# Performance work log

Measured on AMD Instinct MI355X. Metric: run time of the kernel, lower is better.

Reference implementation:

```python
import jax, jax.numpy as jnp
import numpy as np

H = 16          # n_heads
DH = 128        # head_dim
DR = 64         # rope_dim
DC = DH - DR    # content_dim = 64
THETA = 10000.0
SCALE = 1.0 / np.sqrt(DH)


def _rope_tables(T, dtype):
    inv = 1.0 / (THETA ** (jnp.arange(0, DR, 2, dtype=jnp.float32) / DR))  # [DR/2]
    t = jnp.arange(T, dtype=jnp.float32)
    freqs = jnp.outer(t, inv)  # [T, DR/2]
    return jnp.cos(freqs).astype(dtype), jnp.sin(freqs).astype(dtype)


def _apply_rope(x, cos, sin):
    # x: [B,H,T,DR]; cos/sin: [T,DR/2] broadcast over B,H
    d = x.shape[-1] // 2
    x1, x2 = x[..., :d], x[..., d:]
    return jnp.concatenate([x1 * cos - x2 * sin, x1 * sin + x2 * cos], axis=-1)


def setup_inputs() -> dict:
    key = jax.random.key(0)
    ks = jax.random.split(key, 9)
    B, T, D = 1, 2048, 2048
    s = 0.02
    return {
        "x": jax.random.normal(ks[0], (B, T, D), jnp.float32),
        "Wq_down": jax.random.normal(ks[1], (D, 512), jnp.float32) * s,
        "Wq_up": jax.random.normal(ks[2], (512, H * DC), jnp.float32) * s,
        "Wq_rope": jax.random.normal(ks[3], (D, H * DR), jnp.float32) * s,
        "Wkv_down": jax.random.normal(ks[4], (D, 512), jnp.float32) * s,
        "Wk_up": jax.random.normal(ks[5], (512, H * DC), jnp.float32) * s,
        "Wv_up": jax.random.normal(ks[6], (512, H * DH), jnp.float32) * s,
        "Wk_rope": jax.random.normal(ks[7], (D, H * DR), jnp.float32) * s,
        "Wo": jax.random.normal(ks[8], (H * DH, D), jnp.float32) * s,
    }


def reference(x, Wq_down, Wq_up, Wq_rope, Wkv_down, Wk_up, Wv_up, Wk_rope, Wo):
    B, T, D = x.shape
    # low-rank query path: down then up, content part only
    q_content = ((x @ Wq_down) @ Wq_up).reshape(B, T, H, DC).transpose(0, 2, 1, 3)
    q_pos = (x @ Wq_rope).reshape(B, T, H, DR).transpose(0, 2, 1, 3)
    kv_latent = x @ Wkv_down                    # [B,T,d_latent]
    k_pos = (x @ Wk_rope).reshape(B, T, H, DR).transpose(0, 2, 1, 3)

    cos, sin = _rope_tables(T, x.dtype)
    q_pos = _apply_rope(q_pos, cos, sin)
    k_pos = _apply_rope(k_pos, cos, sin)

    k_content = (kv_latent @ Wk_up).reshape(B, T, H, DC).transpose(0, 2, 1, 3)
    v = (kv_latent @ Wv_up).reshape(B, T, H, DH).transpose(0, 2, 1, 3)

    q = jnp.concatenate([q_content, q_pos], axis=-1)  # [B,H,T,DH]
    k = jnp.concatenate([k_content, k_pos], axis=-1)  # [B,H,T,DH]

    scores = jnp.einsum("bhtd,bhsd->bhts", q, k) * SCALE
    causal = jnp.tril(jnp.ones((T, T), dtype=bool))
    scores = jnp.where(causal, scores, jnp.finfo(scores.dtype).min)
    attn = jax.nn.softmax(scores, axis=-1)
    out = jnp.einsum("bhts,bhsd->bhtd", attn, v)       # [B,H,T,DH]
    out = out.transpose(0, 2, 1, 3).reshape(B, T, H * DH)
    return out @ Wo
```

## Files before the change

### kernel.cpp

```cpp
#include <hip/hip_runtime.h>
#include <math.h>

#define T_SEQ 2048
#define D_MODEL 2048
#define H_HEADS 16
#define DH 128
#define DR 64
#define DC 64
#define D_LAT 512
#define NSPLIT 3
#define QSCALE (0.08838834764831845f * 1.4426950408889634f)

typedef __attribute__((ext_vector_type(8))) short short8;
typedef __attribute__((ext_vector_type(4))) short short4v;
typedef __attribute__((ext_vector_type(4))) float f32x4;

__device__ __forceinline__ float bf2f(short b) {
    unsigned u = ((unsigned)(unsigned short)b) << 16;
    return __builtin_bit_cast(float, u);
}
__device__ __forceinline__ short f2bf(float f) {
    unsigned u = __builtin_bit_cast(unsigned, f);
    unsigned r = u + 0x7fffu + ((u >> 16) & 1u);
    return (short)(r >> 16);
}
__device__ __forceinline__ short f2bf_trunc(float f) {
    return (short)(__builtin_bit_cast(unsigned, f) >> 16);
}

#define GLD_LDS(gp, lp) \
    __builtin_amdgcn_global_load_lds( \
        (const __attribute__((address_space(1))) void*)(gp), \
        (__attribute__((address_space(3))) void*)(lp), 16, 0, 0)

__device__ __forceinline__ void ct_tile(float (*tile)[33],
                                        const float* __restrict__ W,
                                        short* __restrict__ Wt,
                                        int R, int C, int ldo, int rel) {
    int bx = rel % (C / 32), by = rel / (C / 32);
    int c0 = bx * 32, r0 = by * 32;
    int tx = threadIdx.x & 31, ty = threadIdx.x >> 5;
    #pragma unroll
    for (int i = 0; i < 4; ++i)
        tile[ty + i * 8][tx] = W[(size_t)(r0 + ty + i * 8) * C + c0 + tx];
    __syncthreads();
    #pragma unroll
    for (int i = 0; i < 4; ++i)
        Wt[(size_t)(c0 + ty + i * 8) * ldo + r0 + tx] = f2bf(tile[tx][ty + i * 8]);
    __syncthreads();
}

__global__ __launch_bounds__(256) void prep(const float* __restrict__ x,
                                            short* __restrict__ xb,
                                            const float* __restrict__ Wqd,
                                            const float* __restrict__ Wkvd,
                                            const float* __restrict__ Wqr,
                                            const float* __restrict__ Wkr,
                                            const float* __restrict__ Wqu,
                                            const float* __restrict__ Wku,
                                            const float* __restrict__ Wvu,
                                            const float* __restrict__ Wo,
                                            short* __restrict__ WdT,
                                            short* __restrict__ WupT2,
                                            short* __restrict__ WoT) {
    __shared__ float tile[32][33];
    int bid = blockIdx.x;
    if (bid < 4096) {
        int i = bid * 1024 + threadIdx.x * 4;
        float4 f = *(const float4*)&x[i];
        short4v o;
        o.x = f2bf(f.x); o.y = f2bf(f.y); o.z = f2bf(f.z); o.w = f2bf(f.w);
        *(short4v*)&xb[i] = o;
    } else if (bid < 5120) {
        ct_tile(tile, Wqd,  WdT + (size_t)0 * 2048,    2048, 512,  2048, bid - 4096);
    } else if (bid < 6144) {
        ct_tile(tile, Wkvd, WdT + (size_t)512 * 2048,  2048, 512,  2048, bid - 5120);
    } else if (bid < 8192) {
        ct_tile(tile, Wqr,  WdT + (size_t)1024 * 2048, 2048, 1024, 2048, bid - 6144);
    } else if (bid < 10240) {
        ct_tile(tile, Wkr,  WdT + (size_t)2048 * 2048, 2048, 1024, 2048, bid - 8192);
    } else if (bid < 10752) {
        ct_tile(tile, Wqu,  WupT2 + (size_t)0 * 512,    512, 1024, 512, bid - 10240);
    } else if (bid < 11264) {
        ct_tile(tile, Wku,  WupT2 + (size_t)1024 * 512, 512, 1024, 512, bid - 10752);
    } else if (bid < 12288) {
        ct_tile(tile, Wvu,  WupT2 + (size_t)2048 * 512, 512, 2048, 512, bid - 11264);
    } else {
        ct_tile(tile, Wo,   WoT, 2048, 2048, 2048, bid - 12288);
    }
}

__global__ __launch_bounds__(256) void transpose_bf16(const short* __restrict__ in,
                                                      short* __restrict__ outb,
                                                      int ldi) {
    __shared__ short tile[64][65];
    int c0 = blockIdx.x * 64, t0 = blockIdx.y * 64;
    int tx = threadIdx.x & 31, ty = threadIdx.x >> 5;
    #pragma unroll
    for (int i = 0; i < 8; ++i) {
        int r = ty + i * 8;
        int vv = *(const int*)&in[(size_t)(t0 + r) * ldi + c0 + tx * 2];
        tile[r][tx * 2]     = (short)(vv & 0xffff);
        tile[r][tx * 2 + 1] = (short)(((unsigned)vv) >> 16);
    }
    __syncthreads();
    #pragma unroll
    for (int i = 0; i < 8; ++i) {
        int c = ty + i * 8;
        unsigned lo = (unsigned short)tile[tx * 2][c];
        unsigned hi = (unsigned short)tile[tx * 2 + 1][c];
        *(int*)&outb[(size_t)(c0 + c) * 2048 + t0 + tx * 2] = (int)(lo | (hi << 16));
    }
}

__global__ __launch_bounds__(256) void gemm_bt(const short* __restrict__ A,
                                               const short* __restrict__ A2,
                                               const short* __restrict__ Bt,
                                               short* __restrict__ C0,
                                               short* __restrict__ C1,
                                               int M, int N, int Kblk,
                                               int lda, int ldb, int ldc,
                                               int ncut, int scut, float cscale) {
    __shared__ short As[128 * 32];
    __shared__ short Bs[128 * 32];
    const int tid = threadIdx.x;
    const int wave = tid >> 6, lane = tid & 63;
    const int row0 = blockIdx.y * 128, col0 = blockIdx.x * 128;
    const int kbase = blockIdx.z * Kblk;
    const short* Ause = (col0 < ncut) ? A : A2;
    short* Cuse = blockIdx.z ? C1 : C0;
    const int wr = (wave >> 1) * 64, wc = (wave & 1) * 64;
    const int lr = lane & 15, quad = lane >> 4;

    f32x4 acc[4][4];
    #pragma unroll
    for (int i = 0; i < 4; ++i)
        #pragma unroll
        for (int j = 0; j < 4; ++j) acc[i][j] = (f32x4){0.f, 0.f, 0.f, 0.f};

    for (int k0 = kbase; k0 < kbase + Kblk; k0 += 32) {
        __syncthreads();
        #pragma unroll
        for (int it = 0; it < 2; ++it) {
            int idx = wave * 64 + it * 256 + lane;
            const short* ga = Ause + (size_t)(row0 + (idx >> 2)) * lda + k0 + (idx & 3) * 8;
            const short* gb = Bt   + (size_t)(col0 + (idx >> 2)) * ldb + k0 + (idx & 3) * 8;
            int lds0 = (wave * 64 + it * 256) * 8;
            GLD_LDS(ga, &As[lds0]);
            GLD_LDS(gb, &Bs[lds0]);
        }
        __syncthreads();

        short8 af[4], bfr[4];
        #pragma unroll
        for (int i = 0; i < 4; ++i)
            af[i] = *(const short8*)&As[(wr + i * 16 + lr) * 32 + quad * 8];
        #pragma unroll
        for (int j = 0; j < 4; ++j)
            bfr[j] = *(const short8*)&Bs[(wc + j * 16 + lr) * 32 + quad * 8];
        #pragma unroll
        for (int i = 0; i < 4; ++i)
            #pragma unroll
            for (int j = 0; j < 4; ++j)
                acc[i][j] = __builtin_amdgcn_mfma_f32_16x16x32_bf16(af[i], bfr[j],
                                                                   acc[i][j], 0, 0, 0);
    }

    const float sc = (col0 < scut) ? cscale : 1.0f;
    #pragma unroll
    for (int i = 0; i < 4; ++i) {
        int rb = row0 + wr + i * 16 + quad * 4;
        #pragma unroll
        for (int j = 0; j < 4; ++j) {
            int c = col0 + wc + j * 16 + lr;
            #pragma unroll
            for (int r = 0; r < 4; ++r)
                Cuse[(size_t)(rb + r) * ldc + c] = f2bf(acc[i][j][r] * sc);
        }
    }
}

__global__ __launch_bounds__(256) void add_bf16(short* __restrict__ a,
                                                const short* __restrict__ b) {
    int i = (blockIdx.x * 256 + threadIdx.x) * 8;
    short8 av = *(const short8*)&a[i];
    short8 bv = *(const short8*)&b[i];
    short8 o;
    #pragma unroll
    for (int j = 0; j < 8; ++j) o[j] = f2bf(bf2f(av[j]) + bf2f(bv[j]));
    *(short8*)&a[i] = o;
}

__global__ __launch_bounds__(256) void add_out_f32(const short* __restrict__ p0,
                                                   const short* __restrict__ p1,
                                                   float* __restrict__ out) {
    int i = (blockIdx.x * 256 + threadIdx.x) * 4;
    short4v a = *(const short4v*)&p0[i];
    short4v b = *(const short4v*)&p1[i];
    float4 o;
    o.x = bf2f(a.x) + bf2f(b.x);
    o.y = bf2f(a.y) + bf2f(b.y);
    o.z = bf2f(a.z) + bf2f(b.z);
    o.w = bf2f(a.w) + bf2f(b.w);
    *(float4*)&out[i] = o;
}

__global__ __launch_bounds__(256) void rope_cat(short* __restrict__ cat) {
    int idx = blockIdx.x * 256 + threadIdx.x;
    int i = idx & 31;
    int h = (idx >> 5) & (H_HEADS - 1);
    int t = (idx >> 9) & (T_SEQ - 1);
    int which = idx >> 20;
    size_t base = (size_t)t * 3072 + 1024 + which * 1024 + h * DR;
    float x1 = bf2f(cat[base + i]);
    float x2 = bf2f(cat[base + 32 + i]);
    float freq = (float)t * __powf(10000.0f, -(float)i / 32.0f);
    float c = cosf(freq), s = sinf(freq);
    float sc = which ? 1.0f : QSCALE;
    cat[base + i]      = f2bf((x1 * c - x2 * s) * sc);
    cat[base + 32 + i] = f2bf((x1 * s + x2 * c) * sc);
}

__global__ __launch_bounds__(256) void attn_mla_split(const short* __restrict__ qkup,
                                                      const short* __restrict__ cat,
                                                      const short* __restrict__ vT,
                                                      short* __restrict__ Opart01,
                                                      short* __restrict__ Opart2,
                                                      float* __restrict__ lpart) {
    const int p = blockIdx.x;
    const int h = blockIdx.y;
    const int g = blockIdx.z;
    const int tid = threadIdx.x;
    const int wave = tid >> 6, lane = tid & 63;
    const int lr = lane & 15, quad = lane >> 4;

    __shared__ short Ks[32 * 128];
    __shared__ short Vst[128 * 32];
    __shared__ short Ps[4][16 * 40];

    short* Og = (g < 2) ? Opart01 + (size_t)g * (T_SEQ * 2048) : Opart2;
    const short8 ones = {0x3F80, 0x3F80, 0x3F80, 0x3F80,
                         0x3F80, 0x3F80, 0x3F80, 0x3F80};

    for (int rep = 0; rep < 2; ++rep) {
        const int qt = rep ? (31 - p) : p;
        const int Q0 = qt * 64;
        const int qrow0 = Q0 + wave * 16;
        const int nchunk = 2 * qt + 2;
        const int qmax = qrow0 + 15;

        short8 qf[4];
        {
            int t = qrow0 + lr;
            #pragma unroll
            for (int kci = 0; kci < 4; ++kci) {
                const short* src = (kci < 2)
                    ? qkup + (size_t)t * 4096 + h * 64
                    : cat + (size_t)t * 3072 + 1024 + h * 64;
                qf[kci] = *(const short8*)&src[(kci & 1) * 32 + quad * 8];
            }
        }

        f32x4 Oacc[8];
        #pragma unroll
        for (int d = 0; d < 8; ++d) Oacc[d] = (f32x4){0.f, 0.f, 0.f, 0.f};
        f32x4 Lacc = (f32x4){0.f, 0.f, 0.f, 0.f};

        for (int c = g; c < nchunk; c += NSPLIT) {
            const int s0 = c * 32;
            __syncthreads();
            #pragma unroll
            for (int it = 0; it < 2; ++it) {
                int idx = wave * 64 + it * 256 + lane;
                int lds0 = (wave * 64 + it * 256) * 8;
                int key = idx >> 4, ch = idx & 15;
                int cg = ch ^ (key & 15);
                const short* gk = (cg < 8)
                    ? qkup + (size_t)(s0 + key) * 4096 + 1024 + h * 64 + cg * 8
                    : cat + (size_t)(s0 + key) * 3072 + 2048 + h * 64 + (cg - 8) * 8;
                GLD_LDS(gk, &Ks[lds0]);
                int d = idx >> 2, cp = idx & 3;
                int scg = cp ^ (d & 3);
                const short* gv = vT + (size_t)(h * 128 + d) * 2048 + s0 + scg * 8;
                GLD_LDS(gv, &Vst[lds0]);
            }
            __syncthreads();
            if (s0 > qmax) continue;

            f32x4 sacc[2];
            #pragma unroll
            for (int n = 0; n < 2; ++n) {
                sacc[n] = (f32x4){0.f, 0.f, 0.f, 0.f};
                #pragma unroll
                for (int kci = 0; kci < 4; ++kci) {
                    short8 kf = *(const short8*)
                        &Ks[(n * 16 + lr) * 128 + ((kci * 4 + quad) ^ lr) * 8];
                    sacc[n] = __builtin_amdgcn_mfma_f32_16x16x32_bf16(qf[kci], kf,
                                                                     sacc[n], 0, 0, 0);
                }
            }
            if (s0 + 31 > qrow0) {
                #pragma unroll
                for (int r = 0; r < 4; ++r) {
                    int qg = qrow0 + quad * 4 + r;
                    #pragma unroll
                    for (int n = 0; n < 2; ++n) {
                        int s = s0 + n * 16 + lr;
                        sacc[n][r] = (s <= qg) ? sacc[n][r] : -1e30f;
                    }
                }
            }
            #pragma unroll
            for (int r = 0; r < 4; ++r) {
                Ps[wave][(quad * 4 + r) * 40 + lr]      = f2bf_trunc(exp2f(sacc[0][r]));
                Ps[wave][(quad * 4 + r) * 40 + 16 + lr] = f2bf_trunc(exp2f(sacc[1][r]));
            }
            short8 pf = *(const short8*)&Ps[wave][lr * 40 + quad * 8];
            Lacc = __builtin_amdgcn_mfma_f32_16x16x32_bf16(pf, ones, Lacc, 0, 0, 0);
            #pragma unroll
            for (int dt = 0; dt < 8; ++dt) {
                short8 vf = *(const short8*)
                    &Vst[(dt * 16 + lr) * 32 + (quad ^ (lr & 3)) * 8];
                Oacc[dt] = __builtin_amdgcn_mfma_f32_16x16x32_bf16(pf, vf,
                                                                  Oacc[dt], 0, 0, 0);
            }
        }

        #pragma unroll
        for (int r = 0; r < 4; ++r) {
            int t = qrow0 + quad * 4 + r;
            #pragma unroll
            for (int dt = 0; dt < 8; ++dt)
                Og[(size_t)t * 2048 + h * 128 + dt * 16 + lr] = f2bf(Oacc[dt][r]);
        }
        if (lr == 0) {
            #pragma unroll
            for (int r = 0; r < 4; ++r) {
                int t = qrow0 + quad * 4 + r;
                lpart[(size_t)(g * T_SEQ + t) * H_HEADS + h] = Lacc[r];
            }
        }
    }
}

__global__ __launch_bounds__(256) void attn_combine(const short* __restrict__ O01,
                                                    const short* __restrict__ O2,
                                                    const float* __restrict__ lpart,
                                                    short* __restrict__ ao) {
    const int t = blockIdx.x;
    const int h = blockIdx.y * 2 + (threadIdx.x >> 7);
    const int d = threadIdx.x & 127;
    size_t off = (size_t)t * 2048 + h * 128 + d;
    float num = bf2f(O01[off]) + bf2f(O01[(size_t)T_SEQ * 2048 + off]) + bf2f(O2[off]);
    float den = lpart[(size_t)(0 * T_SEQ + t) * H_HEADS + h] +
                lpart[(size_t)(1 * T_SEQ + t) * H_HEADS + h] +
                lpart[(size_t)(2 * T_SEQ + t) * H_HEADS + h];
    ao[off] = f2bf(num / den);
}

extern "C" void kernel_launch(void* const* d_in, const int* in_sizes, int n_in,
                              void* d_out, int out_size, void* d_ws, size_t ws_size,
                              hipStream_t stream) {
    const float* x        = (const float*)d_in[0];
    const float* Wq_down  = (const float*)d_in[1];
    const float* Wq_up    = (const float*)d_in[2];
    const float* Wq_rope  = (const float*)d_in[3];
    const float* Wkv_down = (const float*)d_in[4];
    const float* Wk_up    = (const float*)d_in[5];
    const float* Wv_up    = (const float*)d_in[6];
    const float* Wk_rope  = (const float*)d_in[7];
    const float* Wo       = (const float*)d_in[8];
    float* out = (float*)d_out;

    short* p = (short*)d_ws;
    short* xb     = p; p += (size_t)2048 * 2048;
    short* WoT    = p; p += (size_t)2048 * 2048;
    short* cat    = p; p += (size_t)2048 * 3072;
    short* upcat2 = p; p += (size_t)2048 * 4096;
    short* WdT    = p; p += (size_t)3072 * 2048;
    short* WupT2  = p; p += (size_t)4096 * 512;
    short* vT     = p; p += (size_t)2048 * 2048;
    float* lpart  = (float*)p;
    short* pdown   = upcat2;
    short* aob     = cat;
    short* Opart01 = WdT;
    short* Opart2  = xb;
    short* pw0     = upcat2;
    short* pw1     = upcat2 + (size_t)2048 * 2048;

    prep<<<dim3(16384), 256, 0, stream>>>(x, xb, Wq_down, Wkv_down, Wq_rope,
                                          Wk_rope, Wq_up, Wk_up, Wv_up, Wo,
                                          WdT, WupT2, WoT);

    gemm_bt<<<dim3(24, 16, 2), 256, 0, stream>>>(xb, xb, WdT, cat, pdown,
                                                 2048, 3072, 1024,
                                                 2048, 2048, 3072, 1 << 30, 0, 1.f);
    add_bf16<<<dim3(2048 * 3072 / 2048), 256, 0, stream>>>(cat, pdown);

    rope_cat<<<dim3(2 * T_SEQ * H_HEADS * 32 / 256), 256, 0, stream>>>(cat);

    gemm_bt<<<dim3(32, 16, 1), 256, 0, stream>>>(cat, cat + 512, WupT2,
                                                 upcat2, upcat2,
                                                 2048, 4096, 512,
                                                 3072, 512, 4096, 1024, 1024, QSCALE);

    transpose_bf16<<<dim3(32, 32), 256, 0, stream>>>(upcat2 + 2048, vT, 4096);

    attn_mla_split<<<dim3(16, 16, NSPLIT), 256, 0, stream>>>(upcat2, cat, vT,
                                                             Opart01, Opart2, lpart);
    attn_combine<<<dim3(2048, 8), 256, 0, stream>>>(Opart01, Opart2, lpart, aob);

    gemm_bt<<<dim3(16, 16, 2), 256, 0, stream>>>(aob, aob, WoT, pw0, pw1,
                                                 2048, 2048, 1024,
                                                 2048, 2048, 2048, 1 << 30, 0, 1.f);
    add_out_f32<<<dim3(2048 * 2048 / 1024), 256, 0, stream>>>(pw0, pw1, out);
}
```

Measured before the change: 292.0 us.

## Swizzle block IDs across XCDs and double attention key chunk to 64

All GEMM and attention launches become 1D grids with a manual remap that groups blocks sharing an output row/column band or head onto the same XCD, aiming to improve L2 reuse on the multi-die MI355X. The attention kernel now processes 64-key chunks per iteration instead of 32, halving syncs and load rounds per key. It skips fully masked 16-key subtiles and zero-fills the masked halves of the P tile. LDS use per block roughly doubles, which may lower occupancy.

```diff
diff --git a/kernel.cpp b/kernel.cpp
--- a/kernel.cpp
+++ b/kernel.cpp
@@ -118,17 +118,24 @@
                                                const short* __restrict__ Bt,
                                                short* __restrict__ C0,
                                                short* __restrict__ C1,
-                                               int M, int N, int Kblk,
+                                               int N, int Kblk,
                                                int lda, int ldb, int ldc,
                                                int ncut, int scut, float cscale) {
     __shared__ short As[128 * 32];
     __shared__ short Bs[128 * 32];
     const int tid = threadIdx.x;
     const int wave = tid >> 6, lane = tid & 63;
-    const int row0 = blockIdx.y * 128, col0 = blockIdx.x * 128;
-    const int kbase = blockIdx.z * Kblk;
+    const int lin = blockIdx.x;
+    const int X = N >> 7, Xq = X >> 2;
+    const int xcd = lin & 7;
+    int r = lin >> 3;
+    const int bx = (xcd & 3) * Xq + (r % Xq); r /= Xq;
+    const int by = (xcd >> 2) * 8 + (r & 7);
+    const int bz = r >> 3;
+    const int row0 = by * 128, col0 = bx * 128;
+    const int kbase = bz * Kblk;
     const short* Ause = (col0 < ncut) ? A : A2;
-    short* Cuse = blockIdx.z ? C1 : C0;
+    short* Cuse = bz ? C1 : C0;
     const int wr = (wave >> 1) * 64, wc = (wave & 1) * 64;
     const int lr = lane & 15, quad = lane >> 4;
 
@@ -174,8 +181,8 @@
         for (int j = 0; j < 4; ++j) {
             int c = col0 + wc + j * 16 + lr;
             #pragma unroll
-            for (int r = 0; r < 4; ++r)
-                Cuse[(size_t)(rb + r) * ldc + c] = f2bf(acc[i][j][r] * sc);
+            for (int rr = 0; rr < 4; ++rr)
+                Cuse[(size_t)(rb + rr) * ldc + c] = f2bf(acc[i][j][rr] * sc);
         }
     }
 }
@@ -227,16 +234,20 @@
                                                       short* __restrict__ Opart01,
                                                       short* __restrict__ Opart2,
                                                       float* __restrict__ lpart) {
-    const int p = blockIdx.x;
-    const int h = blockIdx.y;
-    const int g = blockIdx.z;
+    const int lin = blockIdx.x;
+    const int xcd = lin & 7;
+    const int s_ = lin >> 3;
+    const int h = xcd + 8 * (s_ & 1);
+    const int s2 = s_ >> 1;
+    const int p = s2 & 15;
+    const int g = s2 >> 4;
     const int tid = threadIdx.x;
     const int wave = tid >> 6, lane = tid & 63;
     const int lr = lane & 15, quad = lane >> 4;
 
-    __shared__ short Ks[32 * 128];
-    __shared__ short Vst[128 * 32];
-    __shared__ short Ps[4][16 * 40];
+    __shared__ short Ks[64 * 128];
+    __shared__ short Vst[128 * 64];
+    __shared__ short Ps[4][16 * 72];
 
     short* Og = (g < 2) ? Opart01 + (size_t)g * (T_SEQ * 2048) : Opart2;
     const short8 ones = {0x3F80, 0x3F80, 0x3F80, 0x3F80,
@@ -246,7 +257,7 @@
         const int qt = rep ? (31 - p) : p;
         const int Q0 = qt * 64;
         const int qrow0 = Q0 + wave * 16;
-        const int nchunk = 2 * qt + 2;
+        const int npair = qt + 1;
         const int qmax = qrow0 + 15;
 
         short8 qf[4];
@@ -266,11 +277,11 @@
         for (int d = 0; d < 8; ++d) Oacc[d] = (f32x4){0.f, 0.f, 0.f, 0.f};
         f32x4 Lacc = (f32x4){0.f, 0.f, 0.f, 0.f};
 
-        for (int c = g; c < nchunk; c += NSPLIT) {
-            const int s0 = c * 32;
+        for (int j = g; j < npair; j += NSPLIT) {
+            const int s0 = j * 64;
             __syncthreads();
             #pragma unroll
-            for (int it = 0; it < 2; ++it) {
+            for (int it = 0; it < 4; ++it) {
                 int idx = wave * 64 + it * 256 + lane;
                 int lds0 = (wave * 64 + it * 256) * 8;
                 int key = idx >> 4, ch = idx & 15;
@@ -279,50 +290,58 @@
                     ? qkup + (size_t)(s0 + key) * 4096 + 1024 + h * 64 + cg * 8
                     : cat + (size_t)(s0 + key) * 3072 + 2048 + h * 64 + (cg - 8) * 8;
                 GLD_LDS(gk, &Ks[lds0]);
-                int d = idx >> 2, cp = idx & 3;
-                int scg = cp ^ (d & 3);
+                int d = idx >> 3, cp = idx & 7;
+                int scg = cp ^ (d & 7);
                 const short* gv = vT + (size_t)(h * 128 + d) * 2048 + s0 + scg * 8;
                 GLD_LDS(gv, &Vst[lds0]);
             }
             __syncthreads();
             if (s0 > qmax) continue;
 
-            f32x4 sacc[2];
-            #pragma unroll
-            for (int n = 0; n < 2; ++n) {
-                sacc[n] = (f32x4){0.f, 0.f, 0.f, 0.f};
-                #pragma unroll
-                for (int kci = 0; kci < 4; ++kci) {
-                    short8 kf = *(const short8*)
-                        &Ks[(n * 16 + lr) * 128 + ((kci * 4 + quad) ^ lr) * 8];
-                    sacc[n] = __builtin_amdgcn_mfma_f32_16x16x32_bf16(qf[kci], kf,
-                                                                     sacc[n], 0, 0, 0);
+            const bool diag = (s0 + 63 > qrow0);
+            #pragma unroll
+            for (int n = 0; n < 4; ++n) {
+                const bool nact = (s0 + n * 16) <= qmax;
+                const bool cact = (s0 + (n >> 1) * 32) <= qmax;
+                if (nact) {
+                    f32x4 sacc = (f32x4){0.f, 0.f, 0.f, 0.f};
+                    #pragma unroll
+                    for (int kci = 0; kci < 4; ++kci) {
+                        short8 kf = *(const short8*)
+                            &Ks[(n * 16 + lr) * 128 + (((kci * 4 + quad) ^ lr)) * 8];
+                        sacc = __builtin_amdgcn_mfma_f32_16x16x32_bf16(qf[kci], kf,
+                                                                      sacc, 0, 0, 0);
+                    }
+                    if (diag) {
+                        #pragma unroll
+                        for (int r = 0; r < 4; ++r) {
+                            int qg = qrow0 + quad * 4 + r;
+                            int sv = s0 + n * 16 + lr;
+                            sacc[r] = (sv <= qg) ? sacc[r] : -1e30f;
+                        }
+                    }
+                    #pragma unroll
+                    for (int r = 0; r < 4; ++r)
+                        Ps[wave][(quad * 4 + r) * 72 + n * 16 + lr] =
+                            f2bf_trunc(exp2f(sacc[r]));
+                } else if (cact) {
+                    #pragma unroll
+                    for (int r = 0; r < 4; ++r)
+                        Ps[wave][(quad * 4 + r) * 72 + n * 16 + lr] = 0;
                 }
             }
-            if (s0 + 31 > qrow0) {
+            #pragma unroll
+            for (int kc2 = 0; kc2 < 2; ++kc2) {
+                if (s0 + kc2 * 32 > qmax) continue;
+                short8 pf = *(const short8*)&Ps[wave][lr * 72 + kc2 * 32 + quad * 8];
+                Lacc = __builtin_amdgcn_mfma_f32_16x16x32_bf16(pf, ones, Lacc, 0, 0, 0);
                 #pragma unroll
-                for (int r = 0; r < 4; ++r) {
-                    int qg = qrow0 + quad * 4 + r;
-                    #pragma unroll
-                    for (int n = 0; n < 2; ++n) {
-                        int s = s0 + n * 16 + lr;
-                        sacc[n][r] = (s <= qg) ? sacc[n][r] : -1e30f;
-                    }
+                for (int dt = 0; dt < 8; ++dt) {
+                    short8 vf = *(const short8*)
+                        &Vst[(dt * 16 + lr) * 64 + (((kc2 * 4 + quad) ^ (lr & 7))) * 8];
+                    Oacc[dt] = __builtin_amdgcn_mfma_f32_16x16x32_bf16(pf, vf,
+                                                                      Oacc[dt], 0, 0, 0);
                 }
-            }
-            #pragma unroll
-            for (int r = 0; r < 4; ++r) {
-                Ps[wave][(quad * 4 + r) * 40 + lr]      = f2bf_trunc(exp2f(sacc[0][r]));
-                Ps[wave][(quad * 4 + r) * 40 + 16 + lr] = f2bf_trunc(exp2f(sacc[1][r]));
-            }
-            short8 pf = *(const short8*)&Ps[wave][lr * 40 + quad * 8];
-            Lacc = __builtin_amdgcn_mfma_f32_16x16x32_bf16(pf, ones, Lacc, 0, 0, 0);
-            #pragma unroll
-            for (int dt = 0; dt < 8; ++dt) {
-                short8 vf = *(const short8*)
-                    &Vst[(dt * 16 + lr) * 32 + (quad ^ (lr & 3)) * 8];
-                Oacc[dt] = __builtin_amdgcn_mfma_f32_16x16x32_bf16(pf, vf,
-                                                                  Oacc[dt], 0, 0, 0);
             }
         }
 
@@ -392,26 +411,26 @@
                                           Wk_rope, Wq_up, Wk_up, Wv_up, Wo,
                                           WdT, WupT2, WoT);
 
-    gemm_bt<<<dim3(24, 16, 2), 256, 0, stream>>>(xb, xb, WdT, cat, pdown,
-                                                 2048, 3072, 1024,
-                                                 2048, 2048, 3072, 1 << 30, 0, 1.f);
+    gemm_bt<<<dim3(24 * 16 * 2), 256, 0, stream>>>(xb, xb, WdT, cat, pdown,
+                                                   3072, 1024,
+                                                   2048, 2048, 3072, 1 << 30, 0, 1.f);
     add_bf16<<<dim3(2048 * 3072 / 2048), 256, 0, stream>>>(cat, pdown);
 
     rope_cat<<<dim3(2 * T_SEQ * H_HEADS * 32 / 256), 256, 0, stream>>>(cat);
 
-    gemm_bt<<<dim3(32, 16, 1), 256, 0, stream>>>(cat, cat + 512, WupT2,
-                                                 upcat2, upcat2,
-                                                 2048, 4096, 512,
-                                                 3072, 512, 4096, 1024, 1024, QSCALE);
+    gemm_bt<<<dim3(32 * 16 * 1), 256, 0, stream>>>(cat, cat + 512, WupT2,
+                                                   upcat2, upcat2,
+                                                   4096, 512,
+                                                   3072, 512, 4096, 1024, 1024, QSCALE);
 
     transpose_bf16<<<dim3(32, 32), 256, 0, stream>>>(upcat2 + 2048, vT, 4096);
 
-    attn_mla_split<<<dim3(16, 16, NSPLIT), 256, 0, stream>>>(upcat2, cat, vT,
-                                                             Opart01, Opart2, lpart);
+    attn_mla_split<<<dim3(16 * 16 * NSPLIT), 256, 0, stream>>>(upcat2, cat, vT,
+                                                               Opart01, Opart2, lpart);
     attn_combine<<<dim3(2048, 8), 256, 0, stream>>>(Opart01, Opart2, lpart, aob);
 
-    gemm_bt<<<dim3(16, 16, 2), 256, 0, stream>>>(aob, aob, WoT, pw0, pw1,
-                                                 2048, 2048, 1024,
-                                                 2048, 2048, 2048, 1 << 30, 0, 1.f);
+    gemm_bt<<<dim3(16 * 16 * 2), 256, 0, stream>>>(aob, aob, WoT, pw0, pw1,
+                                                   2048, 1024,
+                                                   2048, 2048, 2048, 1 << 30, 0, 1.f);
     add_out_f32<<<dim3(2048 * 2048 / 1024), 256, 0, stream>>>(pw0, pw1, out);
 }
```

After: 296.0 us. Within noise of the previous version (+1.4%).

## Remap GEMM and attention blocks per XCD, split Wo GEMM 4-way over K

Applied to the files above, without the earlier changes.

GEMM and attention launches now use a flat 1D grid. Block indices are remapped so that blocks landing on the same XCD (lin & 7) share nearby row and column tiles or the same head, which should improve L2 reuse. Attention drops the paired-tile loop over two query tiles and launches one block per query tile, ordered longest-first to improve load balance. The output projection is split four ways over K instead of two, giving more parallel blocks. This costs an extra pair of partial buffers reused from WdT, plus more bf16 partial-sum rounding.

```diff
diff --git a/kernel.cpp b/kernel.cpp
--- a/kernel.cpp
+++ b/kernel.cpp
@@ -118,17 +118,26 @@
                                                const short* __restrict__ Bt,
                                                short* __restrict__ C0,
                                                short* __restrict__ C1,
-                                               int M, int N, int Kblk,
+                                               short* __restrict__ C2,
+                                               short* __restrict__ C3,
+                                               int N, int Kblk,
                                                int lda, int ldb, int ldc,
                                                int ncut, int scut, float cscale) {
     __shared__ short As[128 * 32];
     __shared__ short Bs[128 * 32];
     const int tid = threadIdx.x;
     const int wave = tid >> 6, lane = tid & 63;
-    const int row0 = blockIdx.y * 128, col0 = blockIdx.x * 128;
-    const int kbase = blockIdx.z * Kblk;
+    const int lin = blockIdx.x;
+    const int X = N >> 7, Xq = X >> 2;
+    const int xcd = lin & 7;
+    int r = lin >> 3;
+    const int bx = (xcd & 3) * Xq + (r % Xq); r /= Xq;
+    const int by = (xcd >> 2) * 8 + (r & 7);
+    const int bz = r >> 3;
+    const int row0 = by * 128, col0 = bx * 128;
+    const int kbase = bz * Kblk;
     const short* Ause = (col0 < ncut) ? A : A2;
-    short* Cuse = blockIdx.z ? C1 : C0;
+    short* Cuse = (bz == 0) ? C0 : (bz == 1) ? C1 : (bz == 2) ? C2 : C3;
     const int wr = (wave >> 1) * 64, wc = (wave & 1) * 64;
     const int lr = lane & 15, quad = lane >> 4;
 
@@ -174,8 +183,8 @@
         for (int j = 0; j < 4; ++j) {
             int c = col0 + wc + j * 16 + lr;
             #pragma unroll
-            for (int r = 0; r < 4; ++r)
-                Cuse[(size_t)(rb + r) * ldc + c] = f2bf(acc[i][j][r] * sc);
+            for (int rr = 0; rr < 4; ++rr)
+                Cuse[(size_t)(rb + rr) * ldc + c] = f2bf(acc[i][j][rr] * sc);
         }
     }
 }
@@ -193,15 +202,19 @@
 
 __global__ __launch_bounds__(256) void add_out_f32(const short* __restrict__ p0,
                                                    const short* __restrict__ p1,
+                                                   const short* __restrict__ p2,
+                                                   const short* __restrict__ p3,
                                                    float* __restrict__ out) {
     int i = (blockIdx.x * 256 + threadIdx.x) * 4;
     short4v a = *(const short4v*)&p0[i];
     short4v b = *(const short4v*)&p1[i];
+    short4v c = *(const short4v*)&p2[i];
+    short4v d = *(const short4v*)&p3[i];
     float4 o;
-    o.x = bf2f(a.x) + bf2f(b.x);
-    o.y = bf2f(a.y) + bf2f(b.y);
-    o.z = bf2f(a.z) + bf2f(b.z);
-    o.w = bf2f(a.w) + bf2f(b.w);
+    o.x = (bf2f(a.x) + bf2f(b.x)) + (bf2f(c.x) + bf2f(d.x));
+    o.y = (bf2f(a.y) + bf2f(b.y)) + (bf2f(c.y) + bf2f(d.y));
+    o.z = (bf2f(a.z) + bf2f(b.z)) + (bf2f(c.z) + bf2f(d.z));
+    o.w = (bf2f(a.w) + bf2f(b.w)) + (bf2f(c.w) + bf2f(d.w));
     *(float4*)&out[i] = o;
 }
 
@@ -227,9 +240,13 @@
                                                       short* __restrict__ Opart01,
                                                       short* __restrict__ Opart2,
                                                       float* __restrict__ lpart) {
-    const int p = blockIdx.x;
-    const int h = blockIdx.y;
-    const int g = blockIdx.z;
+    const int lin = blockIdx.x;
+    const int xcd = lin & 7;
+    int r_ = lin >> 3;
+    const int h = xcd + 8 * (r_ & 1);
+    r_ >>= 1;
+    const int qt = 31 - (r_ & 31);
+    const int g = r_ >> 5;
     const int tid = threadIdx.x;
     const int wave = tid >> 6, lane = tid & 63;
     const int lr = lane & 15, quad = lane >> 4;
@@ -242,103 +259,100 @@
     const short8 ones = {0x3F80, 0x3F80, 0x3F80, 0x3F80,
                          0x3F80, 0x3F80, 0x3F80, 0x3F80};
 
-    for (int rep = 0; rep < 2; ++rep) {
-        const int qt = rep ? (31 - p) : p;
-        const int Q0 = qt * 64;
-        const int qrow0 = Q0 + wave * 16;
-        const int nchunk = 2 * qt + 2;
-        const int qmax = qrow0 + 15;
-
-        short8 qf[4];
-        {
-            int t = qrow0 + lr;
+    const int Q0 = qt * 64;
+    const int qrow0 = Q0 + wave * 16;
+    const int nchunk = 2 * qt + 2;
+    const int qmax = qrow0 + 15;
+
+    short8 qf[4];
+    {
+        int t = qrow0 + lr;
+        #pragma unroll
+        for (int kci = 0; kci < 4; ++kci) {
+            const short* src = (kci < 2)
+                ? qkup + (size_t)t * 4096 + h * 64
+                : cat + (size_t)t * 3072 + 1024 + h * 64;
+            qf[kci] = *(const short8*)&src[(kci & 1) * 32 + quad * 8];
+        }
+    }
+
+    f32x4 Oacc[8];
+    #pragma unroll
+    for (int d = 0; d < 8; ++d) Oacc[d] = (f32x4){0.f, 0.f, 0.f, 0.f};
+    f32x4 Lacc = (f32x4){0.f, 0.f, 0.f, 0.f};
+
+    for (int c = g; c < nchunk; c += NSPLIT) {
+        const int s0 = c * 32;
+        __syncthreads();
+        #pragma unroll
+        for (int it = 0; it < 2; ++it) {
+            int idx = wave * 64 + it * 256 + lane;
+            int lds0 = (wave * 64 + it * 256) * 8;
+            int key = idx >> 4, ch = idx & 15;
+            int cg = ch ^ (key & 15);
+            const short* gk = (cg < 8)
+                ? qkup + (size_t)(s0 + key) * 4096 + 1024 + h * 64 + cg * 8
+                : cat + (size_t)(s0 + key) * 3072 + 2048 + h * 64 + (cg - 8) * 8;
+            GLD_LDS(gk, &Ks[lds0]);
+            int d = idx >> 2, cp = idx & 3;
+            int scg = cp ^ (d & 3);
+            const short* gv = vT + (size_t)(h * 128 + d) * 2048 + s0 + scg * 8;
+            GLD_LDS(gv, &Vst[lds0]);
+        }
+        __syncthreads();
+        if (s0 > qmax) continue;
+
+        f32x4 sacc[2];
+        #pragma unroll
+        for (int n = 0; n < 2; ++n) {
+            sacc[n] = (f32x4){0.f, 0.f, 0.f, 0.f};
             #pragma unroll
             for (int kci = 0; kci < 4; ++kci) {
-                const short* src = (kci < 2)
-                    ? qkup + (size_t)t * 4096 + h * 64
-                    : cat + (size_t)t * 3072 + 1024 + h * 64;
-                qf[kci] = *(const short8*)&src[(kci & 1) * 32 + quad * 8];
+                short8 kf = *(const short8*)
+                    &Ks[(n * 16 + lr) * 128 + ((kci * 4 + quad) ^ lr) * 8];
+                sacc[n] = __builtin_amdgcn_mfma_f32_16x16x32_bf16(qf[kci], kf,
+                                                                 sacc[n], 0, 0, 0);
             }
         }
-
-        f32x4 Oacc[8];
-        #pragma unroll
-        for (int d = 0; d < 8; ++d) Oacc[d] = (f32x4){0.f, 0.f, 0.f, 0.f};
-        f32x4 Lacc = (f32x4){0.f, 0.f, 0.f, 0.f};
-
-        for (int c = g; c < nchunk; c += NSPLIT) {
-            const int s0 = c * 32;
-            __syncthreads();
+        if (s0 + 31 > qrow0) {
             #pragma unroll
-            for (int it = 0; it < 2; ++it) {
-                int idx = wave * 64 + it * 256 + lane;
-                int lds0 = (wave * 64 + it * 256) * 8;
-                int key = idx >> 4, ch = idx & 15;
-                int cg = ch ^ (key & 15);
-                const short* gk = (cg < 8)
-                    ? qkup + (size_t)(s0 + key) * 4096 + 1024 + h * 64 + cg * 8
-                    : cat + (size_t)(s0 + key) * 3072 + 2048 + h * 64 + (cg - 8) * 8;
-                GLD_LDS(gk, &Ks[lds0]);
-                int d = idx >> 2, cp = idx & 3;
-                int scg = cp ^ (d & 3);
-                const short* gv = vT + (size_t)(h * 128 + d) * 2048 + s0 + scg * 8;
-                GLD_LDS(gv, &Vst[lds0]);
-            }
-            __syncthreads();
-            if (s0 > qmax) continue;
-
-            f32x4 sacc[2];
-            #pragma unroll
-            for (int n = 0; n < 2; ++n) {
-                sacc[n] = (f32x4){0.f, 0.f, 0.f, 0.f};
+            for (int r = 0; r < 4; ++r) {
+                int qg = qrow0 + quad * 4 + r;
                 #pragma unroll
-                for (int kci = 0; kci < 4; ++kci) {
-                    short8 kf = *(const short8*)
-                        &Ks[(n * 16 + lr) * 128 + ((kci * 4 + quad) ^ lr) * 8];
-                    sacc[n] = __builtin_amdgcn_mfma_f32_16x16x32_bf16(qf[kci], kf,
-                                                                     sacc[n], 0, 0, 0);
+                for (int n = 0; n < 2; ++n) {
+                    int s = s0 + n * 16 + lr;
+                    sacc[n][r] = (s <= qg) ? sacc[n][r] : -1e30f;
                 }
             }
-            if (s0 + 31 > qrow0) {
-                #pragma unroll
-                for (int r = 0; r < 4; ++r) {
-                    int qg = qrow0 + quad * 4 + r;
-                    #pragma unroll
-                    for (int n = 0; n < 2; ++n) {
-                        int s = s0 + n * 16 + lr;
-                        sacc[n][r] = (s <= qg) ? sacc[n][r] : -1e30f;
-                    }
-                }
-            }
-            #pragma unroll
-            for (int r = 0; r < 4; ++r) {
-                Ps[wave][(quad * 4 + r) * 40 + lr]      = f2bf_trunc(exp2f(sacc[0][r]));
-                Ps[wave][(quad * 4 + r) * 40 + 16 + lr] = f2bf_trunc(exp2f(sacc[1][r]));
-            }
-            short8 pf = *(const short8*)&Ps[wave][lr * 40 + quad * 8];
-            Lacc = __builtin_amdgcn_mfma_f32_16x16x32_bf16(pf, ones, Lacc, 0, 0, 0);
-            #pragma unroll
-            for (int dt = 0; dt < 8; ++dt) {
-                short8 vf = *(const short8*)
-                    &Vst[(dt * 16 + lr) * 32 + (quad ^ (lr & 3)) * 8];
-                Oacc[dt] = __builtin_amdgcn_mfma_f32_16x16x32_bf16(pf, vf,
-                                                                  Oacc[dt], 0, 0, 0);
-            }
-        }
-
+        }
+        #pragma unroll
+        for (int r = 0; r < 4; ++r) {
+            Ps[wave][(quad * 4 + r) * 40 + lr]      = f2bf_trunc(exp2f(sacc[0][r]));
+            Ps[wave][(quad * 4 + r) * 40 + 16 + lr] = f2bf_trunc(exp2f(sacc[1][r]));
+        }
+        short8 pf = *(const short8*)&Ps[wave][lr * 40 + quad * 8];
+        Lacc = __builtin_amdgcn_mfma_f32_16x16x32_bf16(pf, ones, Lacc, 0, 0, 0);
+        #pragma unroll
+        for (int dt = 0; dt < 8; ++dt) {
+            short8 vf = *(const short8*)
+                &Vst[(dt * 16 + lr) * 32 + (quad ^ (lr & 3)) * 8];
+            Oacc[dt] = __builtin_amdgcn_mfma_f32_16x16x32_bf16(pf, vf,
+                                                              Oacc[dt], 0, 0, 0);
+        }
+    }
+
+    #pragma unroll
+    for (int r = 0; r < 4; ++r) {
+        int t = qrow0 + quad * 4 + r;
+        #pragma unroll
+        for (int dt = 0; dt < 8; ++dt)
+            Og[(size_t)t * 2048 + h * 128 + dt * 16 + lr] = f2bf(Oacc[dt][r]);
+    }
+    if (lr == 0) {
         #pragma unroll
         for (int r = 0; r < 4; ++r) {
             int t = qrow0 + quad * 4 + r;
-            #pragma unroll
-            for (int dt = 0; dt < 8; ++dt)
-                Og[(size_t)t * 2048 + h * 128 + dt * 16 + lr] = f2bf(Oacc[dt][r]);
-        }
-        if (lr == 0) {
-            #pragma unroll
-            for (int r = 0; r < 4; ++r) {
-                int t = qrow0 + quad * 4 + r;
-                lpart[(size_t)(g * T_SEQ + t) * H_HEADS + h] = Lacc[r];
-            }
+            lpart[(size_t)(g * T_SEQ + t) * H_HEADS + h] = Lacc[r];
         }
     }
 }
@@ -387,31 +401,34 @@
     short* Opart2  = xb;
     short* pw0     = upcat2;
     short* pw1     = upcat2 + (size_t)2048 * 2048;
+    short* pw2     = WdT;
+    short* pw3     = WdT + (size_t)2048 * 2048;
 
     prep<<<dim3(16384), 256, 0, stream>>>(x, xb, Wq_down, Wkv_down, Wq_rope,
                                           Wk_rope, Wq_up, Wk_up, Wv_up, Wo,
                                           WdT, WupT2, WoT);
 
-    gemm_bt<<<dim3(24, 16, 2), 256, 0, stream>>>(xb, xb, WdT, cat, pdown,
-                                                 2048, 3072, 1024,
-                                                 2048, 2048, 3072, 1 << 30, 0, 1.f);
+    gemm_bt<<<dim3(24 * 16 * 2), 256, 0, stream>>>(xb, xb, WdT, cat, pdown,
+                                                   nullptr, nullptr,
+                                                   3072, 1024,
+                                                   2048, 2048, 3072, 1 << 30, 0, 1.f);
     add_bf16<<<dim3(2048 * 3072 / 2048), 256, 0, stream>>>(cat, pdown);
 
     rope_cat<<<dim3(2 * T_SEQ * H_HEADS * 32 / 256), 256, 0, stream>>>(cat);
 
-    gemm_bt<<<dim3(32, 16, 1), 256, 0, stream>>>(cat, cat + 512, WupT2,
-                                                 upcat2, upcat2,
-                                                 2048, 4096, 512,
-                                                 3072, 512, 4096, 1024, 1024, QSCALE);
+    gemm_bt<<<dim3(32 * 16 * 1), 256, 0, stream>>>(cat, cat + 512, WupT2,
+                                                   upcat2, nullptr, nullptr, nullptr,
+                                                   4096, 512,
+                                                   3072, 512, 4096, 1024, 1024, QSCALE);
 
     transpose_bf16<<<dim3(32, 32), 256, 0, stream>>>(upcat2 + 2048, vT, 4096);
 
-    attn_mla_split<<<dim3(16, 16, NSPLIT), 256, 0, stream>>>(upcat2, cat, vT,
-                                                             Opart01, Opart2, lpart);
+    attn_mla_split<<<dim3(32 * 16 * NSPLIT), 256, 0, stream>>>(upcat2, cat, vT,
+                                                               Opart01, Opart2, lpart);
     attn_combine<<<dim3(2048, 8), 256, 0, stream>>>(Opart01, Opart2, lpart, aob);
 
-    gemm_bt<<<dim3(16, 16, 2), 256, 0, stream>>>(aob, aob, WoT, pw0, pw1,
-                                                 2048, 2048, 1024,
-                                                 2048, 2048, 2048, 1 << 30, 0, 1.f);
-    add_out_f32<<<dim3(2048 * 2048 / 1024), 256, 0, stream>>>(pw0, pw1, out);
-}
+    gemm_bt<<<dim3(16 * 16 * 4), 256, 0, stream>>>(aob, aob, WoT, pw0, pw1, pw2, pw3,
+                                                   2048, 512,
+                                                   2048, 2048, 2048, 1 << 30, 0, 1.f);
+    add_out_f32<<<dim3(2048 * 2048 / 1024), 256, 0, stream>>>(pw0, pw1, pw2, pw3, out);
+}
```

Result: no change. 294.9 us (+1.0%).
